# Kernel tuning notes

Measured on AMD Instinct MI355X. Metric: run time of the kernel, lower is better.

Reference implementation:

```python
import jax, jax.numpy as jnp
import numpy as np

B = 256          # batch
S = 128 * 128    # s = imwidth*imheight (flattened image)
R = 16           # TT rank
N = 6            # number of TT cores


def setup_inputs() -> dict:
    key = jax.random.key(0)
    ks = jax.random.split(key, N + 1)
    # layeroptions['normalize']: cores divided by sqrt(sqrt(s))
    scale = 0.02 / np.sqrt(np.sqrt(S))
    ranklist = [1] + [R] * (N - 1) + [1]
    inp = {"z": jax.random.normal(ks[0], (B, S), dtype=jnp.float32)}
    for n in range(N):
        inp[f"core{n}"] = (
            jax.random.normal(ks[n + 1], (ranklist[n], S, ranklist[n + 1]), dtype=jnp.float32)
            * scale
        )
    inp["b"] = B
    return inp


def reference(z, core0, core1, core2, core3, core4, core5, b):
    # cores[k] has shape (d1, S, d2) with ranklist = [1, R, ..., R, 1]
    cores = [core0, core1, core2, core3, core4, core5]
    # f starts as TT[0][0] : (S, R)  (first core has d1 == 1)
    f = core0[0]
    # V_k[b] = sum_s z[b, s] * cores[k][:, s, :]   -> (b, d1, d2)
    # (equivalent to matmul(z, TT[k].permute(1,0,2).reshape(S, d1*d2)))
    V1 = jnp.einsum('bs,dse->bde', z, cores[1])          # (B, R, R)
    f = jnp.einsum('sd,bde->bse', f, V1)                 # (B, S, R)
    for k in range(2, N):
        Vk = jnp.einsum('bs,dse->bde', z, cores[k])      # (B, R, d2)
        f = jnp.einsum('bsd,bde->bse', f, Vk)            # (B, S, d2)
    # final d2 == 1 -> (B, S, 1) -> flatten like f.reshape(-1)
    return f.reshape(-1)
```

## Files before the change

### kernel.cpp

```cpp
#include <hip/hip_runtime.h>
#include <cstddef>
#include <cstdint>

namespace {
constexpr int kB = 256;
constexpr int kS = 16384;
constexpr int kNCol = 1040;
constexpr int BK = 64;
}

using short8 = __attribute__((ext_vector_type(8))) short;
using f32x4  = __attribute__((ext_vector_type(4))) float;

__device__ __forceinline__ void cvt4(float x0, float x1, float x2, float x3,
                                     ushort4& h, ushort4& l) {
    uint32_t u0 = __float_as_uint(x0), u1 = __float_as_uint(x1),
             u2 = __float_as_uint(x2), u3 = __float_as_uint(x3);
    h.x = (unsigned short)(u0 >> 16); h.y = (unsigned short)(u1 >> 16);
    h.z = (unsigned short)(u2 >> 16); h.w = (unsigned short)(u3 >> 16);
    float r0 = x0 - __uint_as_float(u0 & 0xffff0000u);
    float r1 = x1 - __uint_as_float(u1 & 0xffff0000u);
    float r2 = x2 - __uint_as_float(u2 & 0xffff0000u);
    float r3 = x3 - __uint_as_float(u3 & 0xffff0000u);
    l.x = (unsigned short)(__float_as_uint(r0) >> 16);
    l.y = (unsigned short)(__float_as_uint(r1) >> 16);
    l.z = (unsigned short)(__float_as_uint(r2) >> 16);
    l.w = (unsigned short)(__float_as_uint(r3) >> 16);
}

__global__ __launch_bounds__(256, 2) void fttv_gemm_mfma(
    const float* __restrict__ z,
    const float* __restrict__ c1, const float* __restrict__ c2,
    const float* __restrict__ c3, const float* __restrict__ c4,
    const float* __restrict__ c5,
    float* __restrict__ vp, int kc)
{
    __shared__ unsigned short As[2 * 128 * 64];
    __shared__ unsigned short Bs[2 * 64 * 64];

    const int nwg = gridDim.x;
    const int q = nwg >> 3, r = nwg & 7;
    const int xcd = blockIdx.x & 7, rest = blockIdx.x >> 3;
    const int v = (xcd < r ? xcd * (q + 1) : r * (q + 1) + (xcd - r) * q) + rest;
    const int sk = v / 34;
    const int rem = v - sk * 34;
    const int mt = rem / 17;
    const int ct = rem - mt * 17;

    const int tid = threadIdx.x;
    const int b0 = mt * 128;
    const int sbeg = sk * kc;

    const int ar = tid >> 4;
    const int ak = (tid & 15) * 4;
    const float* zb = z + (size_t)(b0 + ar) * kS + sbeg + ak;

    const int l = tid & 63, w = tid >> 6;
    const int lr = l & 15, lk = (l >> 4) * 8, swz = (l & 7) << 3;

    f32x4 acc[4][2];
    #pragma unroll
    for (int i = 0; i < 4; ++i)
        #pragma unroll
        for (int j = 0; j < 2; ++j) acc[i][j] = (f32x4){0.f, 0.f, 0.f, 0.f};

    if (ct < 16) {
        const int ci = ct >> 2;
        const float* cp = (ci == 0 ? c1 : ci == 1 ? c2 : ci == 2 ? c3 : c4)
                        + (size_t)(ct & 3) * 4 * ((size_t)kS * 16);
        const int bk0 = (tid & 15) * 4;
        const int bn0 = (tid >> 4) * 4;
        const float* bp = cp + (size_t)(bn0 >> 4) * ((size_t)kS * 16)
                        + (size_t)sbeg * 16 + (bn0 & 15);
        const int moff = (w >> 1) * 64, noff = (w & 1) * 32;

        float4 za[8], bb[4];
        #pragma unroll
        for (int p = 0; p < 8; ++p)
            za[p] = *reinterpret_cast<const float4*>(zb + (size_t)16 * p * kS);
        #pragma unroll
        for (int i = 0; i < 4; ++i)
            bb[i] = *reinterpret_cast<const float4*>(bp + (size_t)(bk0 + i) * 16);

        for (int sb = 0; sb < kc; sb += BK) {
            #pragma unroll
            for (int p = 0; p < 8; ++p) {
                const int rr = ar + 16 * p;
                ushort4 h, lo;
                cvt4(za[p].x, za[p].y, za[p].z, za[p].w, h, lo);
                const int idx = rr * 64 + (ak ^ ((rr & 7) << 3));
                *reinterpret_cast<ushort4*>(&As[idx]) = h;
                *reinterpret_cast<ushort4*>(&As[8192 + idx]) = lo;
            }
            #pragma unroll
            for (int j = 0; j < 4; ++j) {
                const int n = bn0 + j;
                ushort4 h, lo;
                cvt4(reinterpret_cast<const float*>(&bb[0])[j],
                     reinterpret_cast<const float*>(&bb[1])[j],
                     reinterpret_cast<const float*>(&bb[2])[j],
                     reinterpret_cast<const float*>(&bb[3])[j], h, lo);
                const int idx = n * 64 + (bk0 ^ ((n & 7) << 3));
                *reinterpret_cast<ushort4*>(&Bs[idx]) = h;
                *reinterpret_cast<ushort4*>(&Bs[4096 + idx]) = lo;
            }
            __syncthreads();
            if (sb + BK < kc) {
                const int sn = sb + BK;
                #pragma unroll
                for (int p = 0; p < 8; ++p)
                    za[p] = *reinterpret_cast<const float4*>(zb + (size_t)16 * p * kS + sn);
                #pragma unroll
                for (int i = 0; i < 4; ++i)
                    bb[i] = *reinterpret_cast<const float4*>(bp + (size_t)(sn + bk0 + i) * 16);
            }
            #pragma unroll
            for (int kb = 0; kb < 2; ++kb) {
                const int kk = (kb * 32 + lk) ^ swz;
                short8 ah[4], al[4], bh[2], bl[2];
                #pragma unroll
                for (int fm = 0; fm < 4; ++fm) {
                    const int row = moff + fm * 16 + lr;
                    ah[fm] = *reinterpret_cast<const short8*>(&As[row * 64 + kk]);
                    al[fm] = *reinterpret_cast<const short8*>(&As[8192 + row * 64 + kk]);
                }
                #pragma unroll
                for (int fn = 0; fn < 2; ++fn) {
                    const int col = noff + fn * 16 + lr;
                    bh[fn] = *reinterpret_cast<const short8*>(&Bs[col * 64 + kk]);
                    bl[fn] = *reinterpret_cast<const short8*>(&Bs[4096 + col * 64 + kk]);
                }
                #pragma unroll
                for (int fm = 0; fm < 4; ++fm)
                    #pragma unroll
                    for (int fn = 0; fn < 2; ++fn) {
                        acc[fm][fn] = __builtin_amdgcn_mfma_f32_16x16x32_bf16(
                            ah[fm], bh[fn], acc[fm][fn], 0, 0, 0);
                        acc[fm][fn] = __builtin_amdgcn_mfma_f32_16x16x32_bf16(
                            ah[fm], bl[fn], acc[fm][fn], 0, 0, 0);
                        acc[fm][fn] = __builtin_amdgcn_mfma_f32_16x16x32_bf16(
                            al[fm], bh[fn], acc[fm][fn], 0, 0, 0);
                    }
            }
            __syncthreads();
        }
        #pragma unroll
        for (int fm = 0; fm < 4; ++fm)
            #pragma unroll
            for (int fn = 0; fn < 2; ++fn) {
                const int col = ct * 64 + noff + fn * 16 + lr;
                const int brow = b0 + moff + fm * 16 + (l >> 4) * 4;
                *reinterpret_cast<f32x4*>(
                    vp + ((size_t)sk * kNCol + col) * kB + brow) = acc[fm][fn];
            }
    } else {
        const int bn = tid & 15;
        const int bk0 = (tid >> 4) * 4;
        const float* bp = c5 + (size_t)bn * kS + sbeg + bk0;
        const int moff = w * 32;

        float4 za[8], bb;
        #pragma unroll
        for (int p = 0; p < 8; ++p)
            za[p] = *reinterpret_cast<const float4*>(zb + (size_t)16 * p * kS);
        bb = *reinterpret_cast<const float4*>(bp);

        for (int sb = 0; sb < kc; sb += BK) {
            #pragma unroll
            for (int p = 0; p < 8; ++p) {
                const int rr = ar + 16 * p;
                ushort4 h, lo;
                cvt4(za[p].x, za[p].y, za[p].z, za[p].w, h, lo);
                const int idx = rr * 64 + (ak ^ ((rr & 7) << 3));
                *reinterpret_cast<ushort4*>(&As[idx]) = h;
                *reinterpret_cast<ushort4*>(&As[8192 + idx]) = lo;
            }
            {
                ushort4 h, lo;
                cvt4(bb.x, bb.y, bb.z, bb.w, h, lo);
                const int idx = bn * 64 + (bk0 ^ ((bn & 7) << 3));
                *reinterpret_cast<ushort4*>(&Bs[idx]) = h;
                *reinterpret_cast<ushort4*>(&Bs[4096 + idx]) = lo;
            }
            __syncthreads();
            if (sb + BK < kc) {
                const int sn = sb + BK;
                #pragma unroll
                for (int p = 0; p < 8; ++p)
                    za[p] = *reinterpret_cast<const float4*>(zb + (size_t)16 * p * kS + sn);
                bb = *reinterpret_cast<const float4*>(bp + sn);
            }
            #pragma unroll
            for (int kb = 0; kb < 2; ++kb) {
                const int kk = (kb * 32 + lk) ^ swz;
                short8 ah[2], al[2], bh, bl;
                #pragma unroll
                for (int fm = 0; fm < 2; ++fm) {
                    const int row = moff + fm * 16 + lr;
                    ah[fm] = *reinterpret_cast<const short8*>(&As[row * 64 + kk]);
                    al[fm] = *reinterpret_cast<const short8*>(&As[8192 + row * 64 + kk]);
                }
                bh = *reinterpret_cast<const short8*>(&Bs[lr * 64 + kk]);
                bl = *reinterpret_cast<const short8*>(&Bs[4096 + lr * 64 + kk]);
                #pragma unroll
                for (int fm = 0; fm < 2; ++fm) {
                    acc[fm][0] = __builtin_amdgcn_mfma_f32_16x16x32_bf16(
                        ah[fm], bh, acc[fm][0], 0, 0, 0);
                    acc[fm][0] = __builtin_amdgcn_mfma_f32_16x16x32_bf16(
                        ah[fm], bl, acc[fm][0], 0, 0, 0);
                    acc[fm][0] = __builtin_amdgcn_mfma_f32_16x16x32_bf16(
                        al[fm], bh, acc[fm][0], 0, 0, 0);
                }
            }
            __syncthreads();
        }
        #pragma unroll
        for (int fm = 0; fm < 2; ++fm) {
            const int col = 1024 + lr;
            const int brow = b0 + moff + fm * 16 + (l >> 4) * 4;
            *reinterpret_cast<f32x4*>(
                vp + ((size_t)sk * kNCol + col) * kB + brow) = acc[fm][0];
        }
    }
}

__global__ void fttv_reduce(const float* __restrict__ vp, float* __restrict__ v,
                            int splitk)
{
    const int idx = blockIdx.x * 256 + threadIdx.x;
    float s = 0.f;
    for (int k = 0; k < splitk; ++k) s += vp[(size_t)k * kNCol * kB + idx];
    v[idx] = s;
}

__global__ void fttv_chain(const float* __restrict__ v, float* __restrict__ w)
{
    const int b = blockIdx.x;
    const int lane = threadIdx.x;
    const int d = lane & 15;
    float u = v[(size_t)(1024 + d) * kB + b];
    #pragma unroll
    for (int k = 4; k >= 1; --k) {
        float nu = 0.f;
        #pragma unroll
        for (int e = 0; e < 16; ++e) {
            const float ue = __shfl(u, e, 16);
            nu += v[(size_t)((k - 1) * 256 + d * 16 + e) * kB + b] * ue;
        }
        u = nu;
    }
    if (lane < 16) w[b * 16 + d] = u;
}

__global__ __launch_bounds__(256) void fttv_out(
    const float* __restrict__ c0, const float* __restrict__ w,
    float* __restrict__ out)
{
    __shared__ float wl[64][16];
    const int sc = blockIdx.x & 63;
    const int bq = blockIdx.x >> 6;
    const int tid = threadIdx.x;
    const int s = sc * 256 + tid;
    float f0[16];
    #pragma unroll
    for (int q = 0; q < 4; ++q)
        *reinterpret_cast<float4*>(&f0[q * 4]) =
            *reinterpret_cast<const float4*>(c0 + (size_t)s * 16 + q * 4);
    *reinterpret_cast<float4*>(&wl[0][0] + tid * 4) =
        *reinterpret_cast<const float4*>(w + bq * 1024 + tid * 4);
    __syncthreads();
    for (int bb = 0; bb < 64; ++bb) {
        float a = 0.f;
        #pragma unroll
        for (int d = 0; d < 16; ++d) a += f0[d] * wl[bb][d];
        out[(size_t)(bq * 64 + bb) * kS + s] = a;
    }
}

extern "C" void kernel_launch(void* const* d_in, const int* in_sizes, int n_in,
                              void* d_out, int out_size, void* d_ws, size_t ws_size,
                              hipStream_t stream)
{
    (void)in_sizes; (void)n_in; (void)out_size;
    const float* z  = (const float*)d_in[0];
    const float* c0 = (const float*)d_in[1];
    const float* c1 = (const float*)d_in[2];
    const float* c2 = (const float*)d_in[3];
    const float* c3 = (const float*)d_in[4];
    const float* c4 = (const float*)d_in[5];
    const float* c5 = (const float*)d_in[6];
    float* out = (float*)d_out;
    float* ws  = (float*)d_ws;

    int splitk = 32;
    while (splitk > 1 &&
           ((size_t)(splitk + 1) * kNCol * kB + (size_t)kB * 16) * sizeof(float) > ws_size)
        splitk >>= 1;
    const int kc = kS / splitk;

    float* vp = ws;
    float* v  = vp + (size_t)splitk * kNCol * kB;
    float* w  = v + (size_t)kNCol * kB;

    fttv_gemm_mfma<<<dim3(34 * splitk), 256, 0, stream>>>(z, c1, c2, c3, c4, c5, vp, kc);
    fttv_reduce<<<dim3((kNCol * kB) / 256), 256, 0, stream>>>(vp, v, splitk);
    fttv_chain<<<dim3(kB), 64, 0, stream>>>(v, w);
    fttv_out<<<dim3(256), 256, 0, stream>>>(c0, w, out);
}
```

Measured before the change: 73.11 us.

## Widen GEMM N-tile to 128 with 32x32 MFMA and row-major partials

The split-K GEMM now gives each workgroup 128 output columns instead of 64, cutting the grid from 34 to 18 tiles per K-split so each z tile is loaded and converted to bf16 hi/lo fewer times. The main path switches to 32x32x16 bf16 MFMA with 16-wide accumulators, and z is loaded as contiguous row segments converted eight at a time. The partial-sum layout changes from column-major to batch-major, which changes the GEMM's scalar epilogue stores and the chain kernel's reads. Risks include uncoalesced scalar stores in the epilogue, higher register use per thread, and fewer workgroups to fill the device.

```diff
diff --git a/kernel.cpp b/kernel.cpp
--- a/kernel.cpp
+++ b/kernel.cpp
@@ -9,8 +9,9 @@
 constexpr int BK = 64;
 }
 
-using short8 = __attribute__((ext_vector_type(8))) short;
-using f32x4  = __attribute__((ext_vector_type(4))) float;
+using short8  = __attribute__((ext_vector_type(8))) short;
+using f32x4   = __attribute__((ext_vector_type(4))) float;
+using f32x16  = __attribute__((ext_vector_type(16))) float;
 
 __device__ __forceinline__ void cvt4(float x0, float x1, float x2, float x3,
                                      ushort4& h, ushort4& l) {
@@ -28,6 +29,18 @@
     l.w = (unsigned short)(__float_as_uint(r3) >> 16);
 }
 
+__device__ __forceinline__ void cvt8(const float4& a, const float4& b,
+                                     short8& h, short8& l) {
+    float x[8] = {a.x, a.y, a.z, a.w, b.x, b.y, b.z, b.w};
+    #pragma unroll
+    for (int i = 0; i < 8; ++i) {
+        uint32_t u = __float_as_uint(x[i]);
+        h[i] = (short)(u >> 16);
+        float r = x[i] - __uint_as_float(u & 0xffff0000u);
+        l[i] = (short)(__float_as_uint(r) >> 16);
+    }
+}
+
 __global__ __launch_bounds__(256, 2) void fttv_gemm_mfma(
     const float* __restrict__ z,
     const float* __restrict__ c1, const float* __restrict__ c2,
@@ -35,191 +48,209 @@
     const float* __restrict__ c5,
     float* __restrict__ vp, int kc)
 {
-    __shared__ unsigned short As[2 * 128 * 64];
-    __shared__ unsigned short Bs[2 * 64 * 64];
+    __shared__ __align__(16) unsigned short As[2 * 128 * 64];
+    __shared__ __align__(16) unsigned short Bs[2 * 128 * 64];
 
     const int nwg = gridDim.x;
     const int q = nwg >> 3, r = nwg & 7;
     const int xcd = blockIdx.x & 7, rest = blockIdx.x >> 3;
-    const int v = (xcd < r ? xcd * (q + 1) : r * (q + 1) + (xcd - r) * q) + rest;
-    const int sk = v / 34;
-    const int rem = v - sk * 34;
-    const int mt = rem / 17;
-    const int ct = rem - mt * 17;
+    const int vfl = (xcd < r ? xcd * (q + 1) : r * (q + 1) + (xcd - r) * q) + rest;
+    const int sk = vfl / 18;
+    const int rem = vfl - sk * 18;
+    const int mt = rem / 9;
+    const int ct = rem - mt * 9;
 
     const int tid = threadIdx.x;
+    const int w = tid >> 6, l = tid & 63;
+    const int wm = w >> 1, wn = w & 1;
     const int b0 = mt * 128;
     const int sbeg = sk * kc;
 
-    const int ar = tid >> 4;
-    const int ak = (tid & 15) * 4;
-    const float* zb = z + (size_t)(b0 + ar) * kS + sbeg + ak;
-
-    const int l = tid & 63, w = tid >> 6;
-    const int lr = l & 15, lk = (l >> 4) * 8, swz = (l & 7) << 3;
-
-    f32x4 acc[4][2];
-    #pragma unroll
-    for (int i = 0; i < 4; ++i)
-        #pragma unroll
-        for (int j = 0; j < 2; ++j) acc[i][j] = (f32x4){0.f, 0.f, 0.f, 0.f};
-
-    if (ct < 16) {
-        const int ci = ct >> 2;
-        const float* cp = (ci == 0 ? c1 : ci == 1 ? c2 : ci == 2 ? c3 : c4)
-                        + (size_t)(ct & 3) * 4 * ((size_t)kS * 16);
+    const int arow = tid >> 1;
+    const int ak0 = (tid & 1) * 32;
+    const float* zp = z + (size_t)(b0 + arow) * kS + sbeg + ak0;
+    const int aswz = (arow & 7) << 3;
+
+    if (ct < 8) {
+        const int ci = ct >> 1;
+        const float* cp = (ci == 0 ? c1 : ci == 1 ? c2 : ci == 2 ? c3 : c4);
+        const int bn0 = (tid >> 4) * 8;
         const int bk0 = (tid & 15) * 4;
-        const int bn0 = (tid >> 4) * 4;
-        const float* bp = cp + (size_t)(bn0 >> 4) * ((size_t)kS * 16)
-                        + (size_t)sbeg * 16 + (bn0 & 15);
-        const int moff = (w >> 1) * 64, noff = (w & 1) * 32;
-
-        float4 za[8], bb[4];
+        const int off = (ct & 1) * 128 + bn0;
+        const int d0 = off >> 4, e0 = off & 15;
+        const float* bp = cp + (size_t)d0 * kS * 16 + e0;
+
+        f32x16 acc[2][2];
+        #pragma unroll
+        for (int i = 0; i < 2; ++i)
+            #pragma unroll
+            for (int j = 0; j < 2; ++j)
+                #pragma unroll
+                for (int t = 0; t < 16; ++t) acc[i][j][t] = 0.f;
+
+        float4 za[8], bb0[4], bb1[4];
         #pragma unroll
         for (int p = 0; p < 8; ++p)
-            za[p] = *reinterpret_cast<const float4*>(zb + (size_t)16 * p * kS);
-        #pragma unroll
-        for (int i = 0; i < 4; ++i)
-            bb[i] = *reinterpret_cast<const float4*>(bp + (size_t)(bk0 + i) * 16);
+            za[p] = *reinterpret_cast<const float4*>(zp + 4 * p);
+        #pragma unroll
+        for (int j = 0; j < 4; ++j) {
+            const size_t so = (size_t)(sbeg + bk0 + j) * 16;
+            bb0[j] = *reinterpret_cast<const float4*>(bp + so);
+            bb1[j] = *reinterpret_cast<const float4*>(bp + so + 4);
+        }
 
         for (int sb = 0; sb < kc; sb += BK) {
             #pragma unroll
-            for (int p = 0; p < 8; ++p) {
-                const int rr = ar + 16 * p;
+            for (int p2 = 0; p2 < 4; ++p2) {
+                short8 h, lo;
+                cvt8(za[2 * p2], za[2 * p2 + 1], h, lo);
+                const int kx = (ak0 + p2 * 8) ^ aswz;
+                *reinterpret_cast<short8*>(&As[arow * 64 + kx]) = h;
+                *reinterpret_cast<short8*>(&As[8192 + arow * 64 + kx]) = lo;
+            }
+            #pragma unroll
+            for (int j = 0; j < 8; ++j) {
+                const float4* src = (j < 4) ? bb0 : bb1;
+                const int jj = j & 3;
                 ushort4 h, lo;
-                cvt4(za[p].x, za[p].y, za[p].z, za[p].w, h, lo);
-                const int idx = rr * 64 + (ak ^ ((rr & 7) << 3));
-                *reinterpret_cast<ushort4*>(&As[idx]) = h;
-                *reinterpret_cast<ushort4*>(&As[8192 + idx]) = lo;
-            }
-            #pragma unroll
-            for (int j = 0; j < 4; ++j) {
-                const int n = bn0 + j;
-                ushort4 h, lo;
-                cvt4(reinterpret_cast<const float*>(&bb[0])[j],
-                     reinterpret_cast<const float*>(&bb[1])[j],
-                     reinterpret_cast<const float*>(&bb[2])[j],
-                     reinterpret_cast<const float*>(&bb[3])[j], h, lo);
-                const int idx = n * 64 + (bk0 ^ ((n & 7) << 3));
-                *reinterpret_cast<ushort4*>(&Bs[idx]) = h;
-                *reinterpret_cast<ushort4*>(&Bs[4096 + idx]) = lo;
+                cvt4(src[0][jj], src[1][jj], src[2][jj], src[3][jj], h, lo);
+                const int col = bn0 + j;
+                const int kx = bk0 ^ ((col & 7) << 3);
+                *reinterpret_cast<ushort4*>(&Bs[col * 64 + kx]) = h;
+                *reinterpret_cast<ushort4*>(&Bs[8192 + col * 64 + kx]) = lo;
             }
             __syncthreads();
             if (sb + BK < kc) {
                 const int sn = sb + BK;
                 #pragma unroll
                 for (int p = 0; p < 8; ++p)
-                    za[p] = *reinterpret_cast<const float4*>(zb + (size_t)16 * p * kS + sn);
-                #pragma unroll
-                for (int i = 0; i < 4; ++i)
-                    bb[i] = *reinterpret_cast<const float4*>(bp + (size_t)(sn + bk0 + i) * 16);
-            }
-            #pragma unroll
-            for (int kb = 0; kb < 2; ++kb) {
-                const int kk = (kb * 32 + lk) ^ swz;
-                short8 ah[4], al[4], bh[2], bl[2];
-                #pragma unroll
-                for (int fm = 0; fm < 4; ++fm) {
-                    const int row = moff + fm * 16 + lr;
-                    ah[fm] = *reinterpret_cast<const short8*>(&As[row * 64 + kk]);
-                    al[fm] = *reinterpret_cast<const short8*>(&As[8192 + row * 64 + kk]);
+                    za[p] = *reinterpret_cast<const float4*>(zp + sn + 4 * p);
+                #pragma unroll
+                for (int j = 0; j < 4; ++j) {
+                    const size_t so = (size_t)(sbeg + sn + bk0 + j) * 16;
+                    bb0[j] = *reinterpret_cast<const float4*>(bp + so);
+                    bb1[j] = *reinterpret_cast<const float4*>(bp + so + 4);
+                }
+            }
+            #pragma unroll
+            for (int ks = 0; ks < 4; ++ks) {
+                const int kf = ks * 16 + (l >> 5) * 8;
+                short8 ah[2], alo[2], bh[2], blo[2];
+                #pragma unroll
+                for (int fm = 0; fm < 2; ++fm) {
+                    const int row = wm * 64 + fm * 32 + (l & 31);
+                    const int kx = kf ^ ((row & 7) << 3);
+                    ah[fm]  = *reinterpret_cast<const short8*>(&As[row * 64 + kx]);
+                    alo[fm] = *reinterpret_cast<const short8*>(&As[8192 + row * 64 + kx]);
                 }
                 #pragma unroll
                 for (int fn = 0; fn < 2; ++fn) {
-                    const int col = noff + fn * 16 + lr;
-                    bh[fn] = *reinterpret_cast<const short8*>(&Bs[col * 64 + kk]);
-                    bl[fn] = *reinterpret_cast<const short8*>(&Bs[4096 + col * 64 + kk]);
-                }
-                #pragma unroll
-                for (int fm = 0; fm < 4; ++fm)
+                    const int col = wn * 64 + fn * 32 + (l & 31);
+                    const int kx = kf ^ ((col & 7) << 3);
+                    bh[fn]  = *reinterpret_cast<const short8*>(&Bs[col * 64 + kx]);
+                    blo[fn] = *reinterpret_cast<const short8*>(&Bs[8192 + col * 64 + kx]);
+                }
+                #pragma unroll
+                for (int fm = 0; fm < 2; ++fm)
                     #pragma unroll
                     for (int fn = 0; fn < 2; ++fn) {
-                        acc[fm][fn] = __builtin_amdgcn_mfma_f32_16x16x32_bf16(
+                        acc[fm][fn] = __builtin_amdgcn_mfma_f32_32x32x16_bf16(
                             ah[fm], bh[fn], acc[fm][fn], 0, 0, 0);
-                        acc[fm][fn] = __builtin_amdgcn_mfma_f32_16x16x32_bf16(
-                            ah[fm], bl[fn], acc[fm][fn], 0, 0, 0);
-                        acc[fm][fn] = __builtin_amdgcn_mfma_f32_16x16x32_bf16(
-                            al[fm], bh[fn], acc[fm][fn], 0, 0, 0);
+                        acc[fm][fn] = __builtin_amdgcn_mfma_f32_32x32x16_bf16(
+                            ah[fm], blo[fn], acc[fm][fn], 0, 0, 0);
+                        acc[fm][fn] = __builtin_amdgcn_mfma_f32_32x32x16_bf16(
+                            alo[fm], bh[fn], acc[fm][fn], 0, 0, 0);
                     }
             }
             __syncthreads();
         }
         #pragma unroll
-        for (int fm = 0; fm < 4; ++fm)
+        for (int fm = 0; fm < 2; ++fm)
             #pragma unroll
             for (int fn = 0; fn < 2; ++fn) {
-                const int col = ct * 64 + noff + fn * 16 + lr;
-                const int brow = b0 + moff + fm * 16 + (l >> 4) * 4;
-                *reinterpret_cast<f32x4*>(
-                    vp + ((size_t)sk * kNCol + col) * kB + brow) = acc[fm][fn];
+                const int rb = b0 + wm * 64 + fm * 32 + 4 * (l >> 5);
+                const int col = ct * 128 + wn * 64 + fn * 32 + (l & 31);
+                #pragma unroll
+                for (int qq = 0; qq < 16; ++qq) {
+                    const int b = rb + (qq & 3) + 8 * (qq >> 2);
+                    vp[((size_t)sk * kB + b) * kNCol + col] = acc[fm][fn][qq];
+                }
             }
     } else {
-        const int bn = tid & 15;
-        const int bk0 = (tid >> 4) * 4;
-        const float* bp = c5 + (size_t)bn * kS + sbeg + bk0;
-        const int moff = w * 32;
-
-        float4 za[8], bb;
+        const int col5 = tid >> 4;
+        const int k05 = (tid & 15) * 4;
+        const float* bp = c5 + (size_t)col5 * kS + sbeg + k05;
+
+        f32x4 acc4[2];
+        #pragma unroll
+        for (int i = 0; i < 2; ++i) acc4[i] = (f32x4){0.f, 0.f, 0.f, 0.f};
+
+        float4 za[8], bz;
         #pragma unroll
         for (int p = 0; p < 8; ++p)
-            za[p] = *reinterpret_cast<const float4*>(zb + (size_t)16 * p * kS);
-        bb = *reinterpret_cast<const float4*>(bp);
+            za[p] = *reinterpret_cast<const float4*>(zp + 4 * p);
+        bz = *reinterpret_cast<const float4*>(bp);
 
         for (int sb = 0; sb < kc; sb += BK) {
             #pragma unroll
-            for (int p = 0; p < 8; ++p) {
-                const int rr = ar + 16 * p;
-                ushort4 h, lo;
-                cvt4(za[p].x, za[p].y, za[p].z, za[p].w, h, lo);
-                const int idx = rr * 64 + (ak ^ ((rr & 7) << 3));
-                *reinterpret_cast<ushort4*>(&As[idx]) = h;
-                *reinterpret_cast<ushort4*>(&As[8192 + idx]) = lo;
+            for (int p2 = 0; p2 < 4; ++p2) {
+                short8 h, lo;
+                cvt8(za[2 * p2], za[2 * p2 + 1], h, lo);
+                const int kx = (ak0 + p2 * 8) ^ aswz;
+                *reinterpret_cast<short8*>(&As[arow * 64 + kx]) = h;
+                *reinterpret_cast<short8*>(&As[8192 + arow * 64 + kx]) = lo;
             }
             {
                 ushort4 h, lo;
-                cvt4(bb.x, bb.y, bb.z, bb.w, h, lo);
-                const int idx = bn * 64 + (bk0 ^ ((bn & 7) << 3));
-                *reinterpret_cast<ushort4*>(&Bs[idx]) = h;
-                *reinterpret_cast<ushort4*>(&Bs[4096 + idx]) = lo;
+                cvt4(bz.x, bz.y, bz.z, bz.w, h, lo);
+                const int kx = k05 ^ ((col5 & 7) << 3);
+                *reinterpret_cast<ushort4*>(&Bs[col5 * 64 + kx]) = h;
+                *reinterpret_cast<ushort4*>(&Bs[8192 + col5 * 64 + kx]) = lo;
             }
             __syncthreads();
             if (sb + BK < kc) {
                 const int sn = sb + BK;
                 #pragma unroll
                 for (int p = 0; p < 8; ++p)
-                    za[p] = *reinterpret_cast<const float4*>(zb + (size_t)16 * p * kS + sn);
-                bb = *reinterpret_cast<const float4*>(bp + sn);
+                    za[p] = *reinterpret_cast<const float4*>(zp + sn + 4 * p);
+                bz = *reinterpret_cast<const float4*>(bp + sn);
             }
             #pragma unroll
             for (int kb = 0; kb < 2; ++kb) {
-                const int kk = (kb * 32 + lk) ^ swz;
-                short8 ah[2], al[2], bh, bl;
+                const int kf = kb * 32 + (l >> 4) * 8;
+                short8 ah[2], alo[2], bh, blo;
                 #pragma unroll
                 for (int fm = 0; fm < 2; ++fm) {
-                    const int row = moff + fm * 16 + lr;
-                    ah[fm] = *reinterpret_cast<const short8*>(&As[row * 64 + kk]);
-                    al[fm] = *reinterpret_cast<const short8*>(&As[8192 + row * 64 + kk]);
-                }
-                bh = *reinterpret_cast<const short8*>(&Bs[lr * 64 + kk]);
-                bl = *reinterpret_cast<const short8*>(&Bs[4096 + lr * 64 + kk]);
+                    const int row = w * 32 + fm * 16 + (l & 15);
+                    const int kx = kf ^ ((row & 7) << 3);
+                    ah[fm]  = *reinterpret_cast<const short8*>(&As[row * 64 + kx]);
+                    alo[fm] = *reinterpret_cast<const short8*>(&As[8192 + row * 64 + kx]);
+                }
+                {
+                    const int cc = l & 15;
+                    const int kx = kf ^ ((cc & 7) << 3);
+                    bh  = *reinterpret_cast<const short8*>(&Bs[cc * 64 + kx]);
+                    blo = *reinterpret_cast<const short8*>(&Bs[8192 + cc * 64 + kx]);
+                }
                 #pragma unroll
                 for (int fm = 0; fm < 2; ++fm) {
-                    acc[fm][0] = __builtin_amdgcn_mfma_f32_16x16x32_bf16(
-                        ah[fm], bh, acc[fm][0], 0, 0, 0);
-                    acc[fm][0] = __builtin_amdgcn_mfma_f32_16x16x32_bf16(
-                        ah[fm], bl, acc[fm][0], 0, 0, 0);
-                    acc[fm][0] = __builtin_amdgcn_mfma_f32_16x16x32_bf16(
-                        al[fm], bh, acc[fm][0], 0, 0, 0);
+                    acc4[fm] = __builtin_amdgcn_mfma_f32_16x16x32_bf16(
+                        ah[fm], bh, acc4[fm], 0, 0, 0);
+                    acc4[fm] = __builtin_amdgcn_mfma_f32_16x16x32_bf16(
+                        ah[fm], blo, acc4[fm], 0, 0, 0);
+                    acc4[fm] = __builtin_amdgcn_mfma_f32_16x16x32_bf16(
+                        alo[fm], bh, acc4[fm], 0, 0, 0);
                 }
             }
             __syncthreads();
         }
         #pragma unroll
         for (int fm = 0; fm < 2; ++fm) {
-            const int col = 1024 + lr;
-            const int brow = b0 + moff + fm * 16 + (l >> 4) * 4;
-            *reinterpret_cast<f32x4*>(
-                vp + ((size_t)sk * kNCol + col) * kB + brow) = acc[fm][0];
+            const int rb = b0 + w * 32 + fm * 16 + (l >> 4) * 4;
+            const int col = 1024 + (l & 15);
+            #pragma unroll
+            for (int qq = 0; qq < 4; ++qq)
+                vp[((size_t)sk * kB + rb + qq) * kNCol + col] = acc4[fm][qq];
         }
     }
 }
@@ -236,16 +267,17 @@
 __global__ void fttv_chain(const float* __restrict__ v, float* __restrict__ w)
 {
     const int b = blockIdx.x;
+    const float* vb = v + (size_t)b * kNCol;
     const int lane = threadIdx.x;
     const int d = lane & 15;
-    float u = v[(size_t)(1024 + d) * kB + b];
+    float u = vb[1024 + d];
     #pragma unroll
     for (int k = 4; k >= 1; --k) {
         float nu = 0.f;
         #pragma unroll
         for (int e = 0; e < 16; ++e) {
             const float ue = __shfl(u, e, 16);
-            nu += v[(size_t)((k - 1) * 256 + d * 16 + e) * kB + b] * ue;
+            nu += vb[(k - 1) * 256 + d * 16 + e] * ue;
         }
         u = nu;
     }
@@ -302,7 +334,7 @@
     float* v  = vp + (size_t)splitk * kNCol * kB;
     float* w  = v + (size_t)kNCol * kB;
 
-    fttv_gemm_mfma<<<dim3(34 * splitk), 256, 0, stream>>>(z, c1, c2, c3, c4, c5, vp, kc);
+    fttv_gemm_mfma<<<dim3(18 * splitk), 256, 0, stream>>>(z, c1, c2, c3, c4, c5, vp, kc);
     fttv_reduce<<<dim3((kNCol * kB) / 256), 256, 0, stream>>>(vp, v, splitk);
     fttv_chain<<<dim3(kB), 64, 0, stream>>>(v, w);
     fttv_out<<<dim3(256), 256, 0, stream>>>(c0, w, out);
```

New measurement: 82.86 us. 1.13x slower.

## Replace LDS-staged split-bf16 GEMM with register-direct MFMA operand loads

Applied to the files above, without the earlier changes.

The GEMM kernel no longer stages z and core tiles through shared memory with barriers. Each wave now loads its MFMA fragments straight from global memory into registers, converts them to hi/lo bf16 pairs, and covers all 256 batch rows per block, which halves the grid and enlarges the per-wave tile to 4x4. The partial-sum layout is transposed to batch-major, and the reduce and chain kernels change to match, with the reduce now vectorised to float4. This drops LDS traffic and syncs, but the core loads become strided scalar loads, z gets less reuse across waves, and the transposed epilogue writes are scattered.

```diff
diff --git a/kernel.cpp b/kernel.cpp
--- a/kernel.cpp
+++ b/kernel.cpp
@@ -6,220 +6,172 @@
 constexpr int kB = 256;
 constexpr int kS = 16384;
 constexpr int kNCol = 1040;
-constexpr int BK = 64;
 }
 
 using short8 = __attribute__((ext_vector_type(8))) short;
 using f32x4  = __attribute__((ext_vector_type(4))) float;
 
-__device__ __forceinline__ void cvt4(float x0, float x1, float x2, float x3,
-                                     ushort4& h, ushort4& l) {
-    uint32_t u0 = __float_as_uint(x0), u1 = __float_as_uint(x1),
-             u2 = __float_as_uint(x2), u3 = __float_as_uint(x3);
-    h.x = (unsigned short)(u0 >> 16); h.y = (unsigned short)(u1 >> 16);
-    h.z = (unsigned short)(u2 >> 16); h.w = (unsigned short)(u3 >> 16);
-    float r0 = x0 - __uint_as_float(u0 & 0xffff0000u);
-    float r1 = x1 - __uint_as_float(u1 & 0xffff0000u);
-    float r2 = x2 - __uint_as_float(u2 & 0xffff0000u);
-    float r3 = x3 - __uint_as_float(u3 & 0xffff0000u);
-    l.x = (unsigned short)(__float_as_uint(r0) >> 16);
-    l.y = (unsigned short)(__float_as_uint(r1) >> 16);
-    l.z = (unsigned short)(__float_as_uint(r2) >> 16);
-    l.w = (unsigned short)(__float_as_uint(r3) >> 16);
-}
-
-__global__ __launch_bounds__(256, 2) void fttv_gemm_mfma(
+__device__ __forceinline__ void cvt8r(const float* __restrict__ x,
+                                      short8& h, short8& l) {
+    #pragma unroll
+    for (int i = 0; i < 8; ++i) {
+        uint32_t u = __float_as_uint(x[i]);
+        h[i] = (short)(u >> 16);
+        float r = x[i] - __uint_as_float(u & 0xffff0000u);
+        l[i] = (short)(__float_as_uint(r) >> 16);
+    }
+}
+
+__global__ __launch_bounds__(256, 2) void fttv_gemm_reg(
     const float* __restrict__ z,
     const float* __restrict__ c1, const float* __restrict__ c2,
     const float* __restrict__ c3, const float* __restrict__ c4,
     const float* __restrict__ c5,
     float* __restrict__ vp, int kc)
 {
-    __shared__ unsigned short As[2 * 128 * 64];
-    __shared__ unsigned short Bs[2 * 64 * 64];
-
     const int nwg = gridDim.x;
     const int q = nwg >> 3, r = nwg & 7;
     const int xcd = blockIdx.x & 7, rest = blockIdx.x >> 3;
-    const int v = (xcd < r ? xcd * (q + 1) : r * (q + 1) + (xcd - r) * q) + rest;
-    const int sk = v / 34;
-    const int rem = v - sk * 34;
-    const int mt = rem / 17;
-    const int ct = rem - mt * 17;
-
-    const int tid = threadIdx.x;
-    const int b0 = mt * 128;
-    const int sbeg = sk * kc;
-
-    const int ar = tid >> 4;
-    const int ak = (tid & 15) * 4;
-    const float* zb = z + (size_t)(b0 + ar) * kS + sbeg + ak;
-
-    const int l = tid & 63, w = tid >> 6;
-    const int lr = l & 15, lk = (l >> 4) * 8, swz = (l & 7) << 3;
-
-    f32x4 acc[4][2];
+    const int vfl = (xcd < r ? xcd * (q + 1) : r * (q + 1) + (xcd - r) * q) + rest;
+    const int sk = vfl / 17;
+    const int cg = vfl - sk * 17;
+
+    const int tid = threadIdx.x, w = tid >> 6, l = tid & 63;
+    const int lr = l & 15;
+    const int lk = (l >> 4) * 8;
+    const int row0 = w * 64;
+    const int kbeg = sk * kc;
+
+    const float* za[4];
+    #pragma unroll
+    for (int fm = 0; fm < 4; ++fm)
+        za[fm] = z + (size_t)(row0 + fm * 16 + lr) * kS + kbeg + lk;
+
+    f32x4 acc[4][4];
     #pragma unroll
     for (int i = 0; i < 4; ++i)
         #pragma unroll
-        for (int j = 0; j < 2; ++j) acc[i][j] = (f32x4){0.f, 0.f, 0.f, 0.f};
-
-    if (ct < 16) {
-        const int ci = ct >> 2;
-        const float* cp = (ci == 0 ? c1 : ci == 1 ? c2 : ci == 2 ? c3 : c4)
-                        + (size_t)(ct & 3) * 4 * ((size_t)kS * 16);
-        const int bk0 = (tid & 15) * 4;
-        const int bn0 = (tid >> 4) * 4;
-        const float* bp = cp + (size_t)(bn0 >> 4) * ((size_t)kS * 16)
-                        + (size_t)sbeg * 16 + (bn0 & 15);
-        const int moff = (w >> 1) * 64, noff = (w & 1) * 32;
-
-        float4 za[8], bb[4];
-        #pragma unroll
-        for (int p = 0; p < 8; ++p)
-            za[p] = *reinterpret_cast<const float4*>(zb + (size_t)16 * p * kS);
-        #pragma unroll
-        for (int i = 0; i < 4; ++i)
-            bb[i] = *reinterpret_cast<const float4*>(bp + (size_t)(bk0 + i) * 16);
-
-        for (int sb = 0; sb < kc; sb += BK) {
-            #pragma unroll
-            for (int p = 0; p < 8; ++p) {
-                const int rr = ar + 16 * p;
-                ushort4 h, lo;
-                cvt4(za[p].x, za[p].y, za[p].z, za[p].w, h, lo);
-                const int idx = rr * 64 + (ak ^ ((rr & 7) << 3));
-                *reinterpret_cast<ushort4*>(&As[idx]) = h;
-                *reinterpret_cast<ushort4*>(&As[8192 + idx]) = lo;
-            }
-            #pragma unroll
-            for (int j = 0; j < 4; ++j) {
-                const int n = bn0 + j;
-                ushort4 h, lo;
-                cvt4(reinterpret_cast<const float*>(&bb[0])[j],
-                     reinterpret_cast<const float*>(&bb[1])[j],
-                     reinterpret_cast<const float*>(&bb[2])[j],
-                     reinterpret_cast<const float*>(&bb[3])[j], h, lo);
-                const int idx = n * 64 + (bk0 ^ ((n & 7) << 3));
-                *reinterpret_cast<ushort4*>(&Bs[idx]) = h;
-                *reinterpret_cast<ushort4*>(&Bs[4096 + idx]) = lo;
-            }
-            __syncthreads();
-            if (sb + BK < kc) {
-                const int sn = sb + BK;
-                #pragma unroll
-                for (int p = 0; p < 8; ++p)
-                    za[p] = *reinterpret_cast<const float4*>(zb + (size_t)16 * p * kS + sn);
-                #pragma unroll
-                for (int i = 0; i < 4; ++i)
-                    bb[i] = *reinterpret_cast<const float4*>(bp + (size_t)(sn + bk0 + i) * 16);
-            }
-            #pragma unroll
-            for (int kb = 0; kb < 2; ++kb) {
-                const int kk = (kb * 32 + lk) ^ swz;
-                short8 ah[4], al[4], bh[2], bl[2];
+        for (int j = 0; j < 4; ++j) acc[i][j] = (f32x4){0.f, 0.f, 0.f, 0.f};
+
+    float ra[4][8];
+
+    if (cg < 16) {
+        const int ci = cg >> 2;
+        const float* cp = (ci == 0 ? c1 : ci == 1 ? c2 : ci == 2 ? c3 : c4);
+        const int d0 = (cg & 3) * 4;
+        const float* bpt[4];
+        #pragma unroll
+        for (int fn = 0; fn < 4; ++fn)
+            bpt[fn] = cp + (size_t)(d0 + fn) * kS * 16
+                    + (size_t)(kbeg + lk) * 16 + lr;
+
+        float rb[4][8];
+        #pragma unroll
+        for (int fm = 0; fm < 4; ++fm) {
+            *reinterpret_cast<float4*>(&ra[fm][0]) =
+                *reinterpret_cast<const float4*>(za[fm]);
+            *reinterpret_cast<float4*>(&ra[fm][4]) =
+                *reinterpret_cast<const float4*>(za[fm] + 4);
+        }
+        #pragma unroll
+        for (int fn = 0; fn < 4; ++fn)
+            #pragma unroll
+            for (int j = 0; j < 8; ++j)
+                rb[fn][j] = bpt[fn][(size_t)j * 16];
+
+        for (int kk = 0; kk < kc; kk += 32) {
+            short8 ah[4], al[4], bh[4], bl[4];
+            #pragma unroll
+            for (int fm = 0; fm < 4; ++fm) cvt8r(ra[fm], ah[fm], al[fm]);
+            #pragma unroll
+            for (int fn = 0; fn < 4; ++fn) cvt8r(rb[fn], bh[fn], bl[fn]);
+            if (kk + 32 < kc) {
                 #pragma unroll
                 for (int fm = 0; fm < 4; ++fm) {
-                    const int row = moff + fm * 16 + lr;
-                    ah[fm] = *reinterpret_cast<const short8*>(&As[row * 64 + kk]);
-                    al[fm] = *reinterpret_cast<const short8*>(&As[8192 + row * 64 + kk]);
+                    *reinterpret_cast<float4*>(&ra[fm][0]) =
+                        *reinterpret_cast<const float4*>(za[fm] + kk + 32);
+                    *reinterpret_cast<float4*>(&ra[fm][4]) =
+                        *reinterpret_cast<const float4*>(za[fm] + kk + 36);
                 }
                 #pragma unroll
-                for (int fn = 0; fn < 2; ++fn) {
-                    const int col = noff + fn * 16 + lr;
-                    bh[fn] = *reinterpret_cast<const short8*>(&Bs[col * 64 + kk]);
-                    bl[fn] = *reinterpret_cast<const short8*>(&Bs[4096 + col * 64 + kk]);
+                for (int fn = 0; fn < 4; ++fn)
+                    #pragma unroll
+                    for (int j = 0; j < 8; ++j)
+                        rb[fn][j] = bpt[fn][(size_t)(kk + 32 + j) * 16];
+            }
+            #pragma unroll
+            for (int fm = 0; fm < 4; ++fm)
+                #pragma unroll
+                for (int fn = 0; fn < 4; ++fn) {
+                    acc[fm][fn] = __builtin_amdgcn_mfma_f32_16x16x32_bf16(
+                        ah[fm], bh[fn], acc[fm][fn], 0, 0, 0);
+                    acc[fm][fn] = __builtin_amdgcn_mfma_f32_16x16x32_bf16(
+                        ah[fm], bl[fn], acc[fm][fn], 0, 0, 0);
+                    acc[fm][fn] = __builtin_amdgcn_mfma_f32_16x16x32_bf16(
+                        al[fm], bh[fn], acc[fm][fn], 0, 0, 0);
                 }
-                #pragma unroll
-                for (int fm = 0; fm < 4; ++fm)
-                    #pragma unroll
-                    for (int fn = 0; fn < 2; ++fn) {
-                        acc[fm][fn] = __builtin_amdgcn_mfma_f32_16x16x32_bf16(
-                            ah[fm], bh[fn], acc[fm][fn], 0, 0, 0);
-                        acc[fm][fn] = __builtin_amdgcn_mfma_f32_16x16x32_bf16(
-                            ah[fm], bl[fn], acc[fm][fn], 0, 0, 0);
-                        acc[fm][fn] = __builtin_amdgcn_mfma_f32_16x16x32_bf16(
-                            al[fm], bh[fn], acc[fm][fn], 0, 0, 0);
-                    }
-            }
-            __syncthreads();
         }
         #pragma unroll
         for (int fm = 0; fm < 4; ++fm)
             #pragma unroll
-            for (int fn = 0; fn < 2; ++fn) {
-                const int col = ct * 64 + noff + fn * 16 + lr;
-                const int brow = b0 + moff + fm * 16 + (l >> 4) * 4;
-                *reinterpret_cast<f32x4*>(
-                    vp + ((size_t)sk * kNCol + col) * kB + brow) = acc[fm][fn];
+            for (int fn = 0; fn < 4; ++fn) {
+                const int col = cg * 64 + fn * 16 + lr;
+                const int brow = row0 + fm * 16 + (l >> 4) * 4;
+                #pragma unroll
+                for (int qq = 0; qq < 4; ++qq)
+                    vp[((size_t)sk * kB + brow + qq) * kNCol + col] =
+                        acc[fm][fn][qq];
             }
     } else {
-        const int bn = tid & 15;
-        const int bk0 = (tid >> 4) * 4;
-        const float* bp = c5 + (size_t)bn * kS + sbeg + bk0;
-        const int moff = w * 32;
-
-        float4 za[8], bb;
-        #pragma unroll
-        for (int p = 0; p < 8; ++p)
-            za[p] = *reinterpret_cast<const float4*>(zb + (size_t)16 * p * kS);
-        bb = *reinterpret_cast<const float4*>(bp);
-
-        for (int sb = 0; sb < kc; sb += BK) {
-            #pragma unroll
-            for (int p = 0; p < 8; ++p) {
-                const int rr = ar + 16 * p;
-                ushort4 h, lo;
-                cvt4(za[p].x, za[p].y, za[p].z, za[p].w, h, lo);
-                const int idx = rr * 64 + (ak ^ ((rr & 7) << 3));
-                *reinterpret_cast<ushort4*>(&As[idx]) = h;
-                *reinterpret_cast<ushort4*>(&As[8192 + idx]) = lo;
-            }
-            {
-                ushort4 h, lo;
-                cvt4(bb.x, bb.y, bb.z, bb.w, h, lo);
-                const int idx = bn * 64 + (bk0 ^ ((bn & 7) << 3));
-                *reinterpret_cast<ushort4*>(&Bs[idx]) = h;
-                *reinterpret_cast<ushort4*>(&Bs[4096 + idx]) = lo;
-            }
-            __syncthreads();
-            if (sb + BK < kc) {
-                const int sn = sb + BK;
-                #pragma unroll
-                for (int p = 0; p < 8; ++p)
-                    za[p] = *reinterpret_cast<const float4*>(zb + (size_t)16 * p * kS + sn);
-                bb = *reinterpret_cast<const float4*>(bp + sn);
-            }
-            #pragma unroll
-            for (int kb = 0; kb < 2; ++kb) {
-                const int kk = (kb * 32 + lk) ^ swz;
-                short8 ah[2], al[2], bh, bl;
-                #pragma unroll
-                for (int fm = 0; fm < 2; ++fm) {
-                    const int row = moff + fm * 16 + lr;
-                    ah[fm] = *reinterpret_cast<const short8*>(&As[row * 64 + kk]);
-                    al[fm] = *reinterpret_cast<const short8*>(&As[8192 + row * 64 + kk]);
+        const float* bpt5 = c5 + (size_t)lr * kS + kbeg + lk;
+        float rb[8];
+        #pragma unroll
+        for (int fm = 0; fm < 4; ++fm) {
+            *reinterpret_cast<float4*>(&ra[fm][0]) =
+                *reinterpret_cast<const float4*>(za[fm]);
+            *reinterpret_cast<float4*>(&ra[fm][4]) =
+                *reinterpret_cast<const float4*>(za[fm] + 4);
+        }
+        *reinterpret_cast<float4*>(&rb[0]) =
+            *reinterpret_cast<const float4*>(bpt5);
+        *reinterpret_cast<float4*>(&rb[4]) =
+            *reinterpret_cast<const float4*>(bpt5 + 4);
+
+        for (int kk = 0; kk < kc; kk += 32) {
+            short8 ah[4], al[4], bh, bl;
+            #pragma unroll
+            for (int fm = 0; fm < 4; ++fm) cvt8r(ra[fm], ah[fm], al[fm]);
+            cvt8r(rb, bh, bl);
+            if (kk + 32 < kc) {
+                #pragma unroll
+                for (int fm = 0; fm < 4; ++fm) {
+                    *reinterpret_cast<float4*>(&ra[fm][0]) =
+                        *reinterpret_cast<const float4*>(za[fm] + kk + 32);
+                    *reinterpret_cast<float4*>(&ra[fm][4]) =
+                        *reinterpret_cast<const float4*>(za[fm] + kk + 36);
                 }
-                bh = *reinterpret_cast<const short8*>(&Bs[lr * 64 + kk]);
-                bl = *reinterpret_cast<const short8*>(&Bs[4096 + lr * 64 + kk]);
-                #pragma unroll
-                for (int fm = 0; fm < 2; ++fm) {
-                    acc[fm][0] = __builtin_amdgcn_mfma_f32_16x16x32_bf16(
-                        ah[fm], bh, acc[fm][0], 0, 0, 0);
-                    acc[fm][0] = __builtin_amdgcn_mfma_f32_16x16x32_bf16(
-                        ah[fm], bl, acc[fm][0], 0, 0, 0);
-                    acc[fm][0] = __builtin_amdgcn_mfma_f32_16x16x32_bf16(
-                        al[fm], bh, acc[fm][0], 0, 0, 0);
-                }
-            }
-            __syncthreads();
-        }
-        #pragma unroll
-        for (int fm = 0; fm < 2; ++fm) {
+                *reinterpret_cast<float4*>(&rb[0]) =
+                    *reinterpret_cast<const float4*>(bpt5 + kk + 32);
+                *reinterpret_cast<float4*>(&rb[4]) =
+                    *reinterpret_cast<const float4*>(bpt5 + kk + 36);
+            }
+            #pragma unroll
+            for (int fm = 0; fm < 4; ++fm) {
+                acc[fm][0] = __builtin_amdgcn_mfma_f32_16x16x32_bf16(
+                    ah[fm], bh, acc[fm][0], 0, 0, 0);
+                acc[fm][0] = __builtin_amdgcn_mfma_f32_16x16x32_bf16(
+                    ah[fm], bl, acc[fm][0], 0, 0, 0);
+                acc[fm][0] = __builtin_amdgcn_mfma_f32_16x16x32_bf16(
+                    al[fm], bh, acc[fm][0], 0, 0, 0);
+            }
+        }
+        #pragma unroll
+        for (int fm = 0; fm < 4; ++fm) {
             const int col = 1024 + lr;
-            const int brow = b0 + moff + fm * 16 + (l >> 4) * 4;
-            *reinterpret_cast<f32x4*>(
-                vp + ((size_t)sk * kNCol + col) * kB + brow) = acc[fm][0];
+            const int brow = row0 + fm * 16 + (l >> 4) * 4;
+            #pragma unroll
+            for (int qq = 0; qq < 4; ++qq)
+                vp[((size_t)sk * kB + brow + qq) * kNCol + col] = acc[fm][0][qq];
         }
     }
 }
@@ -227,25 +179,30 @@
 __global__ void fttv_reduce(const float* __restrict__ vp, float* __restrict__ v,
                             int splitk)
 {
-    const int idx = blockIdx.x * 256 + threadIdx.x;
-    float s = 0.f;
-    for (int k = 0; k < splitk; ++k) s += vp[(size_t)k * kNCol * kB + idx];
-    v[idx] = s;
+    const int i4 = blockIdx.x * 256 + threadIdx.x;
+    float4 s = make_float4(0.f, 0.f, 0.f, 0.f);
+    for (int k = 0; k < splitk; ++k) {
+        const float4 t = *reinterpret_cast<const float4*>(
+            vp + (size_t)k * kNCol * kB + (size_t)i4 * 4);
+        s.x += t.x; s.y += t.y; s.z += t.z; s.w += t.w;
+    }
+    *reinterpret_cast<float4*>(v + (size_t)i4 * 4) = s;
 }
 
 __global__ void fttv_chain(const float* __restrict__ v, float* __restrict__ w)
 {
     const int b = blockIdx.x;
+    const float* vb = v + (size_t)b * kNCol;
     const int lane = threadIdx.x;
     const int d = lane & 15;
-    float u = v[(size_t)(1024 + d) * kB + b];
+    float u = vb[1024 + d];
     #pragma unroll
     for (int k = 4; k >= 1; --k) {
         float nu = 0.f;
         #pragma unroll
         for (int e = 0; e < 16; ++e) {
             const float ue = __shfl(u, e, 16);
-            nu += v[(size_t)((k - 1) * 256 + d * 16 + e) * kB + b] * ue;
+            nu += vb[(k - 1) * 256 + d * 16 + e] * ue;
         }
         u = nu;
     }
@@ -302,8 +259,8 @@
     float* v  = vp + (size_t)splitk * kNCol * kB;
     float* w  = v + (size_t)kNCol * kB;
 
-    fttv_gemm_mfma<<<dim3(34 * splitk), 256, 0, stream>>>(z, c1, c2, c3, c4, c5, vp, kc);
-    fttv_reduce<<<dim3((kNCol * kB) / 256), 256, 0, stream>>>(vp, v, splitk);
+    fttv_gemm_reg<<<dim3(17 * splitk), 256, 0, stream>>>(z, c1, c2, c3, c4, c5, vp, kc);
+    fttv_reduce<<<dim3(kNCol * kB / 1024), 256, 0, stream>>>(vp, v, splitk);
     fttv_chain<<<dim3(kB), 64, 0, stream>>>(v, w);
     fttv_out<<<dim3(256), 256, 0, stream>>>(c0, w, out);
 }
```

After: 87.63 us. 1.2x slower.
